# Kernel optimization log

Hardware: AMD Instinct MI355X
Metric: run time of the kernel (lower is better)

## Reference

```python
import jax, jax.numpy as jnp
import numpy as np

N_STARS = 100000
N_ZERNIKES = 45
BATCH = 2048


def setup_inputs() -> dict:
    key = jax.random.key(0)
    k1, k2, k3 = jax.random.split(key, 3)
    # Observed star positions (unique enough in float32 random draws)
    obs_pos = jax.random.normal(k1, (N_STARS, 2), dtype=jnp.float32) * 1000.0
    # Prior Zernike coefficients per observed star
    zks_prior = jax.random.normal(k2, (N_STARS, N_ZERNIKES), dtype=jnp.float32)
    # Query positions are exact rows of obs_pos (the layer does exact-match search)
    sel = jax.random.randint(k3, (BATCH,), 0, N_STARS)
    positions = obs_pos[sel]
    return {"positions": positions, "obs_pos": obs_pos, "zks_prior": zks_prior}


def reference(positions, obs_pos, zks_prior):
    # Faithful to tf.where(tf.equal(obs_pos, pos))[0, 0]:
    # tf.equal broadcasts (n_stars, 2) == (2,) elementwise; tf.where lists True
    # coords in row-major order; [0, 0] is the row index of the FIRST True
    # element anywhere (x OR y coordinate match). We replicate that exactly by
    # flattening the (n_stars, 2) comparison and taking argmax // 2.
    eq = obs_pos[None, :, :] == positions[:, None, :]          # (B, N, 2) bool
    flat = eq.reshape(eq.shape[0], -1)                          # (B, 2N)
    indices = jnp.argmax(flat, axis=1) // 2                     # first-match row
    batch_zks = zks_prior[indices]                              # (B, n_zernikes)
    return batch_zks[:, :, None, None]                          # (B, n_zernikes, 1, 1)
```

## Files before the change

kernel.cpp:

```cpp
#include <hip/hip_runtime.h>
#include <cstdint>


#define LOG2_TABLE 18
#define TABLE_SIZE (1u << LOG2_TABLE)
#define TABLE_MASK (TABLE_SIZE - 1u)
#define EMPTY_KEY  0xFFFFFFFFu
#define NO_IDX     0xFFFFFFFFu

__device__ __forceinline__ uint32_t hmix(uint32_t x) {
    x ^= x >> 16; x *= 0x7feb352du;
    x ^= x >> 15; x *= 0x846ca68bu;
    x ^= x >> 16;
    return x;
}

__device__ __forceinline__ void ht_insert(uint32_t* __restrict__ keys,
                                          uint32_t* __restrict__ vals,
                                          uint32_t kb, uint32_t idx) {
    uint32_t h = hmix(kb) & TABLE_MASK;
    for (;;) {
        uint32_t k = keys[h];
        if (k == kb) { atomicMin(&vals[h], idx); return; }
        if (k == EMPTY_KEY) {
            uint32_t old = atomicCAS(&keys[h], EMPTY_KEY, kb);
            if (old == EMPTY_KEY || old == kb) { atomicMin(&vals[h], idx); return; }
        }
        h = (h + 1u) & TABLE_MASK;
    }
}

__device__ __forceinline__ uint32_t ht_lookup(const uint32_t* __restrict__ keys,
                                              const uint32_t* __restrict__ vals,
                                              uint32_t kb) {
    uint32_t h = hmix(kb) & TABLE_MASK;
    for (;;) {
        uint32_t k = keys[h];
        if (k == kb) return vals[h];
        if (k == EMPTY_KEY) return NO_IDX;
        h = (h + 1u) & TABLE_MASK;
    }
}

__global__ void build_kernel(const float2* __restrict__ obs,
                             uint32_t* __restrict__ ws, int n_stars) {
    int i = blockIdx.x * blockDim.x + threadIdx.x;
    if (i >= n_stars) return;
    uint32_t* kx = ws;
    uint32_t* vx = ws + TABLE_SIZE;
    uint32_t* ky = ws + 2u * TABLE_SIZE;
    uint32_t* vy = ws + 3u * TABLE_SIZE;
    float2 s = obs[i];
    ht_insert(kx, vx, __float_as_uint(s.x), (uint32_t)i);
    ht_insert(ky, vy, __float_as_uint(s.y), (uint32_t)i);
}

__global__ void probe_gather_kernel(const float2* __restrict__ qpos,
                                    const float* __restrict__ zks,
                                    const uint32_t* __restrict__ ws,
                                    float* __restrict__ out,
                                    int batch, int n_zk) {
    int gid  = blockIdx.x * blockDim.x + threadIdx.x;
    int wid  = gid >> 6;
    int lane = gid & 63;
    if (wid >= batch) return;

    const uint32_t* kx = ws;
    const uint32_t* vx = ws + TABLE_SIZE;
    const uint32_t* ky = ws + 2u * TABLE_SIZE;
    const uint32_t* vy = ws + 3u * TABLE_SIZE;

    float2 q = qpos[wid];
    uint32_t ix = ht_lookup(kx, vx, __float_as_uint(q.x));
    uint32_t iy = ht_lookup(ky, vy, __float_as_uint(q.y));
    uint32_t idx = ix < iy ? ix : iy;
    if (idx == NO_IDX) idx = 0;

    if (lane < n_zk)
        out[(long long)wid * n_zk + lane] = zks[(long long)idx * n_zk + lane];
}

#define SBLOCK 256
#define QCHUNK 512
#define SENTINEL 0x7fffffff

__global__ void init_idx(int* __restrict__ minidx, int batch) {
    int t = blockIdx.x * blockDim.x + threadIdx.x;
    if (t < batch) minidx[t] = SENTINEL;
}

__global__ __launch_bounds__(SBLOCK)
void scan_kernel(const float2* __restrict__ obs,
                 const float2* __restrict__ qpos,
                 int* __restrict__ minidx,
                 int n_stars, int batch) {
    __shared__ float2 q[QCHUNK];
    const int qbase = blockIdx.y * QCHUNK;
    for (int j = threadIdx.x; j < QCHUNK; j += SBLOCK) {
        int qi = qbase + j;
        if (qi < batch) q[j] = qpos[qi];
        else { float nv = __int_as_float(0x7fc00000); q[j] = make_float2(nv, nv); }
    }
    __syncthreads();
    const int i = blockIdx.x * SBLOCK + threadIdx.x;
    float sx, sy;
    if (i < n_stars) { float2 s = obs[i]; sx = s.x; sy = s.y; }
    else { sx = __int_as_float(0x7fc00000); sy = sx; }
    #pragma unroll 8
    for (int j = 0; j < QCHUNK; ++j) {
        float2 Q = q[j];
        if (sx == Q.x || sy == Q.y) atomicMin(&minidx[qbase + j], i);
    }
}

__global__ void gather_kernel(const float* __restrict__ zks,
                              const int* __restrict__ minidx,
                              float* __restrict__ out,
                              int batch, int n_zk) {
    int t = blockIdx.x * blockDim.x + threadIdx.x;
    int total = batch * n_zk;
    if (t >= total) return;
    int b = t / n_zk;
    int k = t - b * n_zk;
    int idx = minidx[b];
    if (idx == SENTINEL) idx = 0;
    out[t] = zks[(long long)idx * n_zk + k];
}

extern "C" void kernel_launch(void* const* d_in, const int* in_sizes, int n_in,
                              void* d_out, int out_size, void* d_ws, size_t ws_size,
                              hipStream_t stream) {
    const float2* qpos = (const float2*)d_in[0];
    const float2* obs  = (const float2*)d_in[1];
    const float*  zks  = (const float*)d_in[2];

    const int batch   = in_sizes[0] / 2;
    const int n_stars = in_sizes[1] / 2;
    const int n_zk    = in_sizes[2] / n_stars;

    float* out = (float*)d_out;

    const size_t table_bytes = (size_t)4 * TABLE_SIZE * sizeof(uint32_t);

    if (ws_size >= table_bytes) {
        uint32_t* ws = (uint32_t*)d_ws;
        hipMemsetAsync(ws, 0xFF, table_bytes, stream);
        build_kernel<<<(n_stars + 255) / 256, 256, 0, stream>>>(obs, ws, n_stars);
        int threads = batch * 64;
        probe_gather_kernel<<<(threads + 255) / 256, 256, 0, stream>>>(
            qpos, zks, ws, out, batch, n_zk);
    } else {
        int* minidx = (int*)d_ws;
        init_idx<<<(batch + 255) / 256, 256, 0, stream>>>(minidx, batch);
        dim3 grid((n_stars + SBLOCK - 1) / SBLOCK, (batch + QCHUNK - 1) / QCHUNK);
        scan_kernel<<<grid, SBLOCK, 0, stream>>>(obs, qpos, minidx, n_stars, batch);
        int total = batch * n_zk;
        gather_kernel<<<(total + 255) / 256, 256, 0, stream>>>(zks, minidx, out,
                                                               batch, n_zk);
    }
}
```

Before: 41.95 us.

## Pack hash table key and index into 64-bit slots with single-CAS insert

Replaces the separate 32-bit key and value arrays with one 64-bit slot per entry (key in the high word, index in the low word), so an insert is a single CAS and a lookup reads one word instead of two. A 64-bit atomicMin on the packed value keeps the smallest index for duplicate keys. The hipMemsetAsync is also replaced by a vectorized clear kernel. The aim is fewer atomics and memory transactions in the build and probe phases, at the cost of relying on 64-bit atomics.

```diff
diff --git a/kernel.cpp b/kernel.cpp
--- a/kernel.cpp
+++ b/kernel.cpp
@@ -5,8 +5,10 @@
 #define LOG2_TABLE 18
 #define TABLE_SIZE (1u << LOG2_TABLE)
 #define TABLE_MASK (TABLE_SIZE - 1u)
-#define EMPTY_KEY  0xFFFFFFFFu
+#define EMPTY64    0xFFFFFFFFFFFFFFFFull
 #define NO_IDX     0xFFFFFFFFu
+
+typedef unsigned long long u64;
 
 __device__ __forceinline__ uint32_t hmix(uint32_t x) {
     x ^= x >> 16; x *= 0x7feb352du;
@@ -15,49 +17,55 @@
     return x;
 }
 
-__device__ __forceinline__ void ht_insert(uint32_t* __restrict__ keys,
-                                          uint32_t* __restrict__ vals,
+__device__ __forceinline__ void ht_insert(u64* __restrict__ tab,
                                           uint32_t kb, uint32_t idx) {
+    u64 pack = ((u64)kb << 32) | (u64)idx;
     uint32_t h = hmix(kb) & TABLE_MASK;
     for (;;) {
-        uint32_t k = keys[h];
-        if (k == kb) { atomicMin(&vals[h], idx); return; }
-        if (k == EMPTY_KEY) {
-            uint32_t old = atomicCAS(&keys[h], EMPTY_KEY, kb);
-            if (old == EMPTY_KEY || old == kb) { atomicMin(&vals[h], idx); return; }
+        u64 cur = tab[h];
+        if ((uint32_t)(cur >> 32) == kb) {
+            atomicMin(&tab[h], pack);
+            return;
+        }
+        if (cur == EMPTY64) {
+            u64 old = atomicCAS(&tab[h], EMPTY64, pack);
+            if (old == EMPTY64) return;
+            if ((uint32_t)(old >> 32) == kb) { atomicMin(&tab[h], pack); return; }
         }
         h = (h + 1u) & TABLE_MASK;
     }
 }
 
-__device__ __forceinline__ uint32_t ht_lookup(const uint32_t* __restrict__ keys,
-                                              const uint32_t* __restrict__ vals,
+__device__ __forceinline__ uint32_t ht_lookup(const u64* __restrict__ tab,
                                               uint32_t kb) {
     uint32_t h = hmix(kb) & TABLE_MASK;
     for (;;) {
-        uint32_t k = keys[h];
-        if (k == kb) return vals[h];
-        if (k == EMPTY_KEY) return NO_IDX;
+        u64 cur = tab[h];
+        if ((uint32_t)(cur >> 32) == kb) return (uint32_t)cur;
+        if (cur == EMPTY64) return NO_IDX;
         h = (h + 1u) & TABLE_MASK;
     }
 }
 
+__global__ void clear_kernel(ulonglong2* __restrict__ ws, int n16) {
+    int t = blockIdx.x * blockDim.x + threadIdx.x;
+    if (t < n16) ws[t] = make_ulonglong2(EMPTY64, EMPTY64);
+}
+
 __global__ void build_kernel(const float2* __restrict__ obs,
-                             uint32_t* __restrict__ ws, int n_stars) {
+                             u64* __restrict__ ws, int n_stars) {
     int i = blockIdx.x * blockDim.x + threadIdx.x;
     if (i >= n_stars) return;
-    uint32_t* kx = ws;
-    uint32_t* vx = ws + TABLE_SIZE;
-    uint32_t* ky = ws + 2u * TABLE_SIZE;
-    uint32_t* vy = ws + 3u * TABLE_SIZE;
+    u64* tx = ws;
+    u64* ty = ws + TABLE_SIZE;
     float2 s = obs[i];
-    ht_insert(kx, vx, __float_as_uint(s.x), (uint32_t)i);
-    ht_insert(ky, vy, __float_as_uint(s.y), (uint32_t)i);
+    ht_insert(tx, __float_as_uint(s.x), (uint32_t)i);
+    ht_insert(ty, __float_as_uint(s.y), (uint32_t)i);
 }
 
 __global__ void probe_gather_kernel(const float2* __restrict__ qpos,
                                     const float* __restrict__ zks,
-                                    const uint32_t* __restrict__ ws,
+                                    const u64* __restrict__ ws,
                                     float* __restrict__ out,
                                     int batch, int n_zk) {
     int gid  = blockIdx.x * blockDim.x + threadIdx.x;
@@ -65,14 +73,12 @@
     int lane = gid & 63;
     if (wid >= batch) return;
 
-    const uint32_t* kx = ws;
-    const uint32_t* vx = ws + TABLE_SIZE;
-    const uint32_t* ky = ws + 2u * TABLE_SIZE;
-    const uint32_t* vy = ws + 3u * TABLE_SIZE;
+    const u64* tx = ws;
+    const u64* ty = ws + TABLE_SIZE;
 
     float2 q = qpos[wid];
-    uint32_t ix = ht_lookup(kx, vx, __float_as_uint(q.x));
-    uint32_t iy = ht_lookup(ky, vy, __float_as_uint(q.y));
+    uint32_t ix = ht_lookup(tx, __float_as_uint(q.x));
+    uint32_t iy = ht_lookup(ty, __float_as_uint(q.y));
     uint32_t idx = ix < iy ? ix : iy;
     if (idx == NO_IDX) idx = 0;
 
@@ -140,11 +146,12 @@
 
     float* out = (float*)d_out;
 
-    const size_t table_bytes = (size_t)4 * TABLE_SIZE * sizeof(uint32_t);
+    const size_t table_bytes = (size_t)2 * TABLE_SIZE * sizeof(u64);
 
     if (ws_size >= table_bytes) {
-        uint32_t* ws = (uint32_t*)d_ws;
-        hipMemsetAsync(ws, 0xFF, table_bytes, stream);
+        u64* ws = (u64*)d_ws;
+        int n16 = (int)(table_bytes / 16);
+        clear_kernel<<<(n16 + 255) / 256, 256, 0, stream>>>((ulonglong2*)ws, n16);
         build_kernel<<<(n_stars + 255) / 256, 256, 0, stream>>>(obs, ws, n_stars);
         int threads = batch * 64;
         probe_gather_kernel<<<(threads + 255) / 256, 256, 0, stream>>>(
```

New measurement: 39.40 us. 1.06x faster.
